# Kernel tuning notes

Measured on AMD Instinct MI355X. Metric: run time of the kernel, lower is better.

## Reference

```python
import jax, jax.numpy as jnp
import numpy as np

D_MODEL, N_EXPERTS, TOP_K, D_FF = 1024, 8, 2, 4096
B, T = 2, 2048


def setup_inputs() -> dict:
    key = jax.random.key(0)
    k1, k2, k3, k4 = jax.random.split(key, 4)
    x = jax.random.normal(k1, (B, T, D_MODEL), dtype=jnp.float32)
    # kaiming-uniform-ish gate init
    bound = np.sqrt(6.0 / D_MODEL)
    gate_w = jax.random.uniform(k2, (D_MODEL, N_EXPERTS), dtype=jnp.float32, minval=-bound, maxval=bound)
    s1 = 1.0 / np.sqrt(D_MODEL)
    s2 = 1.0 / np.sqrt(D_FF)
    w1 = jax.random.normal(k3, (N_EXPERTS, D_MODEL, D_FF), dtype=jnp.float32) * s1
    w2 = jax.random.normal(k4, (N_EXPERTS, D_FF, D_MODEL), dtype=jnp.float32) * s2
    return {"x": x, "gate_w": gate_w, "w1": w1, "w2": w2}


def reference(x, gate_w, w1, w2):
    Bb, Tt, D = x.shape
    E = w1.shape[0]
    # --- router ---
    logits = jnp.einsum('btd,de->bte', x, gate_w)            # (B,T,E)
    top_v, top_i = jax.lax.top_k(logits, TOP_K)               # (B,T,K)
    weights = jax.nn.softmax(top_v, axis=-1)                  # (B,T,K)
    routing_probs = jax.nn.softmax(logits, axis=-1)           # (B,T,E)
    m = routing_probs.mean(axis=(0, 1))                       # (E,)
    aux_loss = (m * m).sum() * E
    # --- dispatch/combine via dense combine matrix ---
    N = Bb * Tt
    flat_x = x.reshape(N, D)
    idx = top_i.reshape(N, TOP_K)
    w = weights.reshape(N, TOP_K)
    # combine[n,e] = sum_k weights[n,k] * [idx[n,k]==e]
    combine = jnp.zeros((N, E), dtype=x.dtype).at[jnp.arange(N)[:, None], idx].add(w)
    # --- experts: Linear -> GELU(exact) -> Linear (HolographicExpert stand-in) ---
    h = jax.nn.gelu(jnp.einsum('nd,edf->enf', flat_x, w1), approximate=False)  # (E,N,ff)
    y = jnp.einsum('enf,efd->end', h, w2)                                       # (E,N,d)
    out = jnp.einsum('ne,end->nd', combine, y).reshape(Bb, Tt, D)
    return out, aux_loss
```

## Files before the change

### kernel.cpp

```cpp
#include <hip/hip_runtime.h>
#include <hip/hip_bf16.h>

#define DM   1024
#define NE   8
#define DFF  4096
#define NTOK 4096

typedef __attribute__((ext_vector_type(8))) short bf16x8;
typedef __attribute__((ext_vector_type(4))) float f32x4;

__device__ __forceinline__ short to_bf16(float f) {
  unsigned u = __float_as_uint(f);
  unsigned r = (u + 0x7fffu + ((u >> 16) & 1u)) >> 16;
  return (short)r;
}

__device__ __forceinline__ void gl16(const void* g, void* l) {
  __builtin_amdgcn_global_load_lds(
      (const __attribute__((address_space(1))) unsigned*)g,
      (__attribute__((address_space(3))) unsigned*)l, 16, 0, 0);
}

#define DSB do { __builtin_amdgcn_s_barrier(); __builtin_amdgcn_sched_barrier(0); } while (0)

__device__ __forceinline__ float fast_gelu(float v) {
  float x  = fabsf(v) * 0.70710678118f;
  float t  = __builtin_amdgcn_rcpf(fmaf(0.3275911f, x, 1.0f));
  float p  = t * fmaf(t, fmaf(t, fmaf(t, fmaf(t, 1.061405429f, -1.453152027f),
                                      1.421413741f), -0.284496736f), 0.254829592f);
  float ex = __expf(-x * x);
  float er = fmaf(-p, ex, 1.0f);
  er = (v < 0.f) ? -er : er;
  return 0.5f * v * (1.0f + er);
}

__global__ __launch_bounds__(256) void router_kernel(
    const float* __restrict__ x, const float* __restrict__ gw,
    int* __restrict__ cnt, float* __restrict__ psum,
    int* __restrict__ pairs, float* __restrict__ pairW)
{
  __shared__ float gws[DM * NE];
  __shared__ float part[3][64][NE];
  const int tid = threadIdx.x;
  for (int i = tid * 4; i < DM * NE; i += 256 * 4)
    *reinterpret_cast<float4*>(&gws[i]) = *reinterpret_cast<const float4*>(&gw[i]);
  __syncthreads();

  const int tok = tid & 63;
  const int q   = tid >> 6;
  const int n   = blockIdx.x * 64 + tok;
  float acc[NE];
#pragma unroll
  for (int e = 0; e < NE; ++e) acc[e] = 0.f;

  const float4* xr = reinterpret_cast<const float4*>(x + (size_t)n * DM + q * 256);
  for (int d4 = 0; d4 < 64; ++d4) {
    float4 v = xr[d4];
    const float* gp = &gws[(q * 256 + d4 * 4) * NE];
    float xv;
#pragma unroll
    for (int dd = 0; dd < 4; ++dd) {
      xv = (dd == 0) ? v.x : (dd == 1) ? v.y : (dd == 2) ? v.z : v.w;
#pragma unroll
      for (int e = 0; e < NE; ++e) acc[e] = fmaf(xv, gp[dd * NE + e], acc[e]);
    }
  }

  if (q) {
#pragma unroll
    for (int e = 0; e < NE; ++e) part[q - 1][tok][e] = acc[e];
  }
  __syncthreads();
  if (q == 0) {
#pragma unroll
    for (int e = 0; e < NE; ++e)
      acc[e] += part[0][tok][e] + part[1][tok][e] + part[2][tok][e];

    float mx = acc[0];
#pragma unroll
    for (int e = 1; e < NE; ++e) mx = fmaxf(mx, acc[e]);
    float p[NE], s = 0.f;
#pragma unroll
    for (int e = 0; e < NE; ++e) { p[e] = expf(acc[e] - mx); s += p[e]; }
    float inv = 1.f / s;
#pragma unroll
    for (int e = 0; e < NE; ++e) {
      float v = p[e] * inv;
#pragma unroll
      for (int o = 32; o > 0; o >>= 1) v += __shfl_xor(v, o);
      if (tok == 0) atomicAdd(&psum[e], v);
    }

    float v0 = -1e30f, v1 = -1e30f; int i0 = 0, i1 = 0;
#pragma unroll
    for (int e = 0; e < NE; ++e) {
      float l = acc[e];
      if (l > v0) { v1 = v0; i1 = i0; v0 = l; i0 = e; }
      else if (l > v1) { v1 = l; i1 = e; }
    }
    float e1 = expf(v1 - v0);
    float den = 1.f + e1;
    pairW[n * 2]     = 1.f / den;
    pairW[n * 2 + 1] = e1 / den;
    int p0 = atomicAdd(&cnt[i0], 1); pairs[i0 * NTOK + p0] = n * 2;
    int p1 = atomicAdd(&cnt[i1], 1); pairs[i1 * NTOK + p1] = n * 2 + 1;
  }
}

__global__ void finalize_kernel(const int* __restrict__ cnt, int* __restrict__ off,
                                const float* __restrict__ psum, float* __restrict__ aux)
{
  if (threadIdx.x == 0 && blockIdx.x == 0) {
    int o = 0;
    for (int e = 0; e < NE; ++e) { off[e] = o; o += cnt[e]; }
    off[NE] = o;
    float a = 0.f;
    for (int e = 0; e < NE; ++e) { float me = psum[e] * (1.f / NTOK); a += me * me; }
    aux[0] = a * (float)NE;
  }
}

__global__ __launch_bounds__(256) void convert_x_kernel(
    const float* __restrict__ x, short* __restrict__ xb)
{
  const int i = (blockIdx.x * 256 + threadIdx.x) * 8;
  float4 a = *reinterpret_cast<const float4*>(&x[i]);
  float4 b = *reinterpret_cast<const float4*>(&x[i + 4]);
  union { short s[8]; bf16x8 v; } p;
  p.s[0]=to_bf16(a.x); p.s[1]=to_bf16(a.y); p.s[2]=to_bf16(a.z); p.s[3]=to_bf16(a.w);
  p.s[4]=to_bf16(b.x); p.s[5]=to_bf16(b.y); p.s[6]=to_bf16(b.z); p.s[7]=to_bf16(b.w);
  *reinterpret_cast<bf16x8*>(&xb[i]) = p.v;
}

__global__ __launch_bounds__(256) void transpose_kernel(
    const float* __restrict__ w1, const float* __restrict__ w2,
    short* __restrict__ w1t, short* __restrict__ w2t)
{
  const int z = blockIdx.z;
  const float* src; short* dst; int R, C, rt, ct;
  if (z < 8) { src = w1 + (size_t)z * DM * DFF; dst = w1t + (size_t)z * DM * DFF;
               R = DM; C = DFF; ct = blockIdx.x; rt = blockIdx.y; }
  else       { src = w2 + (size_t)(z - 8) * DM * DFF; dst = w2t + (size_t)(z - 8) * DM * DFF;
               R = DFF; C = DM; ct = blockIdx.y; rt = blockIdx.x; }
  const int r0b = rt * 128, c0b = ct * 128;

  __shared__ __attribute__((aligned(16))) short t_lds[128 * 128];

  const int tid = threadIdx.x;
  const int rq  = tid >> 4;
  const int cq  = tid & 15;

  float4 f[8][2];
  const float* sp = src + (size_t)(r0b + rq * 8) * C + c0b + cq * 8;
#pragma unroll
  for (int i = 0; i < 8; ++i) {
    f[i][0] = *reinterpret_cast<const float4*>(sp + (size_t)i * C);
    f[i][1] = *reinterpret_cast<const float4*>(sp + (size_t)i * C + 4);
  }

#pragma unroll
  for (int j = 0; j < 8; ++j) {
    float v0 = (j < 4) ? f[0][0][j] : f[0][1][j-4];
    float v1 = (j < 4) ? f[1][0][j] : f[1][1][j-4];
    float v2 = (j < 4) ? f[2][0][j] : f[2][1][j-4];
    float v3 = (j < 4) ? f[3][0][j] : f[3][1][j-4];
    float v4 = (j < 4) ? f[4][0][j] : f[4][1][j-4];
    float v5 = (j < 4) ? f[5][0][j] : f[5][1][j-4];
    float v6 = (j < 4) ? f[6][0][j] : f[6][1][j-4];
    float v7 = (j < 4) ? f[7][0][j] : f[7][1][j-4];
    int4 w;
    asm("v_cvt_pk_bf16_f32 %0, %1, %2" : "=v"(w.x) : "v"(v0), "v"(v1));
    asm("v_cvt_pk_bf16_f32 %0, %1, %2" : "=v"(w.y) : "v"(v2), "v"(v3));
    asm("v_cvt_pk_bf16_f32 %0, %1, %2" : "=v"(w.z) : "v"(v4), "v"(v5));
    asm("v_cvt_pk_bf16_f32 %0, %1, %2" : "=v"(w.w) : "v"(v6), "v"(v7));
    const int lc = cq * 8 + j;
    *reinterpret_cast<int4*>(&t_lds[lc * 128 + ((rq ^ (lc & 15)) << 3)]) = w;
  }
  __syncthreads();

#pragma unroll
  for (int v = 0; v < 2; ++v) {
    const int lc2 = (tid >> 2) + v * 64;
    short* dp = dst + (size_t)(c0b + lc2) * R + r0b;
#pragma unroll
    for (int u = 0; u < 4; ++u) {
      const int k = (tid & 3) + u * 4;
      int4 rd = *reinterpret_cast<const int4*>(&t_lds[lc2 * 128 + ((k ^ (lc2 & 15)) << 3)]);
      *reinterpret_cast<int4*>(dp + k * 8) = rd;
    }
  }
}

#define GEMM_LOOP(NT)                                                              \
  f32x4 acc[4][4];                                                                 \
  _Pragma("unroll") for (int i = 0; i < 4; ++i)                                    \
    _Pragma("unroll") for (int j = 0; j < 4; ++j) acc[i][j] = (f32x4){0.f,0.f,0.f,0.f}; \
  STAGE(0, 0);                                                                     \
  STAGE(1, 32);                                                                    \
  {                                                                                \
    int cur = 0, stg = 2;                                                          \
    for (int t = 0; t < (NT); ++t) {                                               \
      if (t < (NT) - 1) { asm volatile("s_waitcnt vmcnt(4)" ::: "memory"); }       \
      else              { asm volatile("s_waitcnt vmcnt(0)" ::: "memory"); }       \
      DSB;                                                                         \
      if (t + 2 < (NT)) STAGE(stg, (t + 2) * 32);                                  \
      bf16x8 af[4], bfv[4];                                                        \
      _Pragma("unroll") for (int i = 0; i < 4; ++i)                                \
        af[i] = *reinterpret_cast<const bf16x8*>(&As[cur][ab + i * 512]);          \
      _Pragma("unroll") for (int j = 0; j < 4; ++j)                                \
        bfv[j] = *reinterpret_cast<const bf16x8*>(&Bs[cur][bb + j * 512]);         \
      _Pragma("unroll") for (int i = 0; i < 4; ++i)                                \
        _Pragma("unroll") for (int j = 0; j < 4; ++j)                              \
          acc[i][j] = __builtin_amdgcn_mfma_f32_16x16x32_bf16(af[i], bfv[j], acc[i][j], 0, 0, 0); \
      cur = (cur == 2) ? 0 : cur + 1;                                              \
      stg = (stg == 2) ? 0 : stg + 1;                                              \
    }                                                                              \
  }

__global__ __launch_bounds__(256) void gemm1_kernel(
    const short* __restrict__ xb, const short* __restrict__ w1t,
    const int* __restrict__ cnt, const int* __restrict__ off,
    const int* __restrict__ pairs, short* __restrict__ h)
{
  const int wg = (blockIdx.x & 7) * 1024 + (blockIdx.x >> 3);
  const int mt = wg & 31;
  const int ft = (wg >> 5) & 31;
  const int e  = wg >> 10;
  const int M  = cnt[e];
  const int m0 = mt * 128;
  if (m0 >= M) return;
  const int ff0  = ft * 128;
  const int base = off[e];

  __shared__ __attribute__((aligned(16))) short As[3][128 * 32];
  __shared__ __attribute__((aligned(16))) short Bs[3][128 * 32];

  const int tid  = threadIdx.x;
  const int lane = tid & 63;
  const int wv   = tid >> 6;
  const int wm   = wv >> 1;
  const int wn   = wv & 1;

  const short* gA[2]; const short* gB[2]; int ldo[2];
#pragma unroll
  for (int l = 0; l < 2; ++l) {
    const int n   = l * 256 + tid;
    const int p   = n >> 3;
    const int s   = n & 7;
    const int cip = s ^ (p & 7);
    const int row = p * 2 + (cip >> 2);
    const int kch = cip & 3;
    int gi = m0 + row; if (gi > M - 1) gi = M - 1;
    const int tok = pairs[e * NTOK + gi] >> 1;
    gA[l]  = xb + (size_t)tok * DM + kch * 8;
    gB[l]  = w1t + ((size_t)e * DFF + ff0 + row) * DM + kch * 8;
    ldo[l] = n * 8;
  }

#define STAGE(buf, k0) do { \
  gl16(gA[0] + (k0), &As[buf][ldo[0]]); \
  gl16(gA[1] + (k0), &As[buf][ldo[1]]); \
  gl16(gB[0] + (k0), &Bs[buf][ldo[0]]); \
  gl16(gB[1] + (k0), &Bs[buf][ldo[1]]); \
} while (0)

  const int lrw = lane & 15;
  const int sr  = ((((lane & 1) << 2) | (lane >> 4)) ^ ((lane & 15) >> 1)) * 8;
  const int ab  = (wm * 32 + (lrw >> 1)) * 64 + sr;
  const int bb  = (wn * 32 + (lrw >> 1)) * 64 + sr;

  GEMM_LOOP(32)
#undef STAGE

  const int erow0 = m0 + wm * 64 + (lane >> 4) * 4;
  const int ecol0 = ff0 + wn * 64 + (lane & 15);
#pragma unroll
  for (int i = 0; i < 4; ++i) {
#pragma unroll
    for (int r = 0; r < 4; ++r) {
      const int grow = erow0 + i * 16 + r;
      if (grow < M) {
        short* hp = h + (size_t)(base + grow) * DFF + ecol0;
#pragma unroll
        for (int j = 0; j < 4; ++j)
          hp[j * 16] = to_bf16(fast_gelu(acc[i][j][r]));
      }
    }
  }
}

__global__ __launch_bounds__(256) void gemm2_kernel(
    const short* __restrict__ h, const short* __restrict__ w2t,
    const int* __restrict__ cnt, const int* __restrict__ off,
    const int* __restrict__ pairs, const float* __restrict__ pairW,
    float* __restrict__ out)
{
  const int wg = (blockIdx.x & 7) * 256 + (blockIdx.x >> 3);
  const int dt = wg & 7;
  const int mt = (wg >> 3) & 31;
  const int e  = wg >> 8;
  const int M  = cnt[e];
  const int m0 = mt * 128;
  if (m0 >= M) return;
  const int d0   = dt * 128;
  const int base = off[e];

  __shared__ __attribute__((aligned(16))) short As[3][128 * 32];
  __shared__ __attribute__((aligned(16))) short Bs[3][128 * 32];

  const int tid  = threadIdx.x;
  const int lane = tid & 63;
  const int wv   = tid >> 6;
  const int wm   = wv >> 1;
  const int wn   = wv & 1;

  const short* gA[2]; const short* gB[2]; int ldo[2];
#pragma unroll
  for (int l = 0; l < 2; ++l) {
    const int n   = l * 256 + tid;
    const int p   = n >> 3;
    const int s   = n & 7;
    const int cip = s ^ (p & 7);
    const int row = p * 2 + (cip >> 2);
    const int kch = cip & 3;
    int gi = m0 + row; if (gi > M - 1) gi = M - 1;
    gA[l]  = h + (size_t)(base + gi) * DFF + kch * 8;
    gB[l]  = w2t + ((size_t)e * DM + d0 + row) * DFF + kch * 8;
    ldo[l] = n * 8;
  }

#define STAGE(buf, k0) do { \
  gl16(gA[0] + (k0), &As[buf][ldo[0]]); \
  gl16(gA[1] + (k0), &As[buf][ldo[1]]); \
  gl16(gB[0] + (k0), &Bs[buf][ldo[0]]); \
  gl16(gB[1] + (k0), &Bs[buf][ldo[1]]); \
} while (0)

  const int lrw = lane & 15;
  const int sr  = ((((lane & 1) << 2) | (lane >> 4)) ^ ((lane & 15) >> 1)) * 8;
  const int ab  = (wm * 32 + (lrw >> 1)) * 64 + sr;
  const int bb  = (wn * 32 + (lrw >> 1)) * 64 + sr;

  GEMM_LOOP(128)
#undef STAGE

  const int erow0 = m0 + wm * 64 + (lane >> 4) * 4;
  const int ecol0 = d0 + wn * 64 + (lane & 15);
#pragma unroll
  for (int i = 0; i < 4; ++i) {
#pragma unroll
    for (int r = 0; r < 4; ++r) {
      const int grow = erow0 + i * 16 + r;
      if (grow < M) {
        const int pr    = pairs[e * NTOK + grow];
        const float wgt = pairW[pr];
        const int tok   = pr >> 1;
#pragma unroll
        for (int j = 0; j < 4; ++j)
          atomicAdd(&out[(size_t)tok * DM + ecol0 + j * 16], wgt * acc[i][j][r]);
      }
    }
  }
}

extern "C" void kernel_launch(void* const* d_in, const int* in_sizes, int n_in,
                              void* d_out, int out_size, void* d_ws, size_t ws_size,
                              hipStream_t stream)
{
  const float* x  = (const float*)d_in[0];
  const float* gw = (const float*)d_in[1];
  const float* w1 = (const float*)d_in[2];
  const float* w2 = (const float*)d_in[3];
  float* outf = (float*)d_out;

  int*   cnt   = (int*)d_ws;
  int*   off   = cnt + 8;
  float* psum  = (float*)(cnt + 20);
  int*   pairs = (int*)((char*)d_ws + 512);
  float* pairW = (float*)((char*)d_ws + 512 + NE * NTOK * 4);
  short* xb    = (short*)((char*)d_ws + (size_t)(1)  * (1 << 20));
  short* w1t   = (short*)((char*)d_ws + (size_t)(16) * (1 << 20));
  short* w2t   = (short*)((char*)d_ws + (size_t)(80) * (1 << 20));
  short* h     = (short*)((char*)d_ws + (size_t)(144)* (1 << 20));

  hipMemsetAsync(d_ws, 0, 512, stream);
  hipMemsetAsync(d_out, 0, (size_t)out_size * sizeof(float), stream);

  router_kernel<<<NTOK / 64, 256, 0, stream>>>(x, gw, cnt, psum, pairs, pairW);
  finalize_kernel<<<1, 64, 0, stream>>>(cnt, off, psum, outf + (size_t)NTOK * DM);
  convert_x_kernel<<<NTOK * DM / (256 * 8), 256, 0, stream>>>(x, xb);
  transpose_kernel<<<dim3(32, 8, 16), 256, 0, stream>>>(w1, w2, w1t, w2t);
  gemm1_kernel<<<8192, 256, 0, stream>>>(xb, w1t, cnt, off, pairs, h);
  gemm2_kernel<<<2048, 256, 0, stream>>>(h, w2t, cnt, off, pairs, pairW, outf);
}
```

Measured before the change: 388.2 us.

## Deepen GEMM LDS pipeline to four stages with register double-buffered fragments

Raises the LDS ring for both expert GEMMs from three to four stages, so there are three tiles of global prefetch in flight. Fragments for the next k-step are loaded from LDS into a second register set while MFMAs run on the current set, with the loop unrolled by two. The aim is to hide global-load and LDS-read latency behind MFMA work. The cost is 64KB of LDS per block and 32 extra VGPRs, which may reduce occupancy. Correctness also depends on NT being even and on the STAGE slot indexing with &3, which is assumed to be handled.

```diff
diff --git a/kernel.cpp b/kernel.cpp
--- a/kernel.cpp
+++ b/kernel.cpp
@@ -191,30 +191,45 @@
   }
 }
 
+
+#define GFRAG(SET, buf)                                                            \
+  _Pragma("unroll") for (int _i = 0; _i < 4; ++_i)                                 \
+    SET##a[_i] = *reinterpret_cast<const bf16x8*>(&As[buf][ab + _i * 512]);        \
+  _Pragma("unroll") for (int _j = 0; _j < 4; ++_j)                                 \
+    SET##b[_j] = *reinterpret_cast<const bf16x8*>(&Bs[buf][bb + _j * 512]);
+
+#define GMFMA(SET)                                                                 \
+  _Pragma("unroll") for (int _i = 0; _i < 4; ++_i)                                 \
+    _Pragma("unroll") for (int _j = 0; _j < 4; ++_j)                               \
+      acc[_i][_j] = __builtin_amdgcn_mfma_f32_16x16x32_bf16(SET##a[_i], SET##b[_j], acc[_i][_j], 0, 0, 0);
+
+#define GITER(t, NT, RD, USE)                                                      \
+  {                                                                                \
+    if ((t) + 3 < (NT)) STAGE(((t) + 3) & 3, ((t) + 3) * 32);                      \
+    if ((t) + 1 < (NT)) {                                                          \
+      if ((t) + 3 < (NT))      { asm volatile("s_waitcnt vmcnt(8)" ::: "memory"); }\
+      else if ((t) + 2 < (NT)) { asm volatile("s_waitcnt vmcnt(4)" ::: "memory"); }\
+      else                     { asm volatile("s_waitcnt vmcnt(0)" ::: "memory"); }\
+      DSB;                                                                         \
+      GFRAG(RD, ((t) + 1) & 3)                                                     \
+    }                                                                              \
+    GMFMA(USE)                                                                     \
+  }
+
 #define GEMM_LOOP(NT)                                                              \
   f32x4 acc[4][4];                                                                 \
   _Pragma("unroll") for (int i = 0; i < 4; ++i)                                    \
     _Pragma("unroll") for (int j = 0; j < 4; ++j) acc[i][j] = (f32x4){0.f,0.f,0.f,0.f}; \
+  bf16x8 Xa[4], Xb[4], Ya[4], Yb[4];                                               \
   STAGE(0, 0);                                                                     \
   STAGE(1, 32);                                                                    \
-  {                                                                                \
-    int cur = 0, stg = 2;                                                          \
-    for (int t = 0; t < (NT); ++t) {                                               \
-      if (t < (NT) - 1) { asm volatile("s_waitcnt vmcnt(4)" ::: "memory"); }       \
-      else              { asm volatile("s_waitcnt vmcnt(0)" ::: "memory"); }       \
-      DSB;                                                                         \
-      if (t + 2 < (NT)) STAGE(stg, (t + 2) * 32);                                  \
-      bf16x8 af[4], bfv[4];                                                        \
-      _Pragma("unroll") for (int i = 0; i < 4; ++i)                                \
-        af[i] = *reinterpret_cast<const bf16x8*>(&As[cur][ab + i * 512]);          \
-      _Pragma("unroll") for (int j = 0; j < 4; ++j)                                \
-        bfv[j] = *reinterpret_cast<const bf16x8*>(&Bs[cur][bb + j * 512]);         \
-      _Pragma("unroll") for (int i = 0; i < 4; ++i)                                \
-        _Pragma("unroll") for (int j = 0; j < 4; ++j)                              \
-          acc[i][j] = __builtin_amdgcn_mfma_f32_16x16x32_bf16(af[i], bfv[j], acc[i][j], 0, 0, 0); \
-      cur = (cur == 2) ? 0 : cur + 1;                                              \
-      stg = (stg == 2) ? 0 : stg + 1;                                              \
-    }                                                                              \
+  STAGE(2, 64);                                                                    \
+  asm volatile("s_waitcnt vmcnt(8)" ::: "memory");                                 \
+  DSB;                                                                             \
+  GFRAG(X, 0)                                                                      \
+  for (int t = 0; t < (NT); t += 2) {                                              \
+    GITER(t, (NT), Y, X)                                                           \
+    GITER(t + 1, (NT), X, Y)                                                       \
   }
 
 __global__ __launch_bounds__(256) void gemm1_kernel(
@@ -232,8 +247,8 @@
   const int ff0  = ft * 128;
   const int base = off[e];
 
-  __shared__ __attribute__((aligned(16))) short As[3][128 * 32];
-  __shared__ __attribute__((aligned(16))) short Bs[3][128 * 32];
+  __shared__ __attribute__((aligned(16))) short As[4][128 * 32];
+  __shared__ __attribute__((aligned(16))) short Bs[4][128 * 32];
 
   const int tid  = threadIdx.x;
   const int lane = tid & 63;
@@ -305,8 +320,8 @@
   const int d0   = dt * 128;
   const int base = off[e];
 
-  __shared__ __attribute__((aligned(16))) short As[3][128 * 32];
-  __shared__ __attribute__((aligned(16))) short Bs[3][128 * 32];
+  __shared__ __attribute__((aligned(16))) short As[4][128 * 32];
+  __shared__ __attribute__((aligned(16))) short Bs[4][128 * 32];
 
   const int tid  = threadIdx.x;
   const int lane = tid & 63;
```

After: 448.6 us. 1.16x slower.
